# Kernel optimization log

Measured on AMD Instinct MI355X. Metric: run time of the kernel, lower is better.

## Reference

```python
import jax, jax.numpy as jnp
import numpy as np

B, T, HID = 2, 2048, 2048
H, KVH, D = 16, 4, 128


def _rope_tables(t, d):
    inv_freq = 1.0 / (10000.0 ** (np.arange(0, d, 2, dtype=np.float32) / d))
    freqs = np.arange(t, dtype=np.float32)[:, None] * inv_freq[None, :]  # [T, d/2]
    emb = np.concatenate([freqs, freqs], axis=-1)  # [T, d]
    return jnp.asarray(np.cos(emb))[None], jnp.asarray(np.sin(emb))[None]  # [1,T,d]


def setup_inputs() -> dict:
    key = jax.random.key(0)
    ks = jax.random.split(key, 5)
    x = jax.random.normal(ks[0], (B, T, HID), dtype=jnp.float32)
    rope_cos, rope_sin = _rope_tables(T, D)
    s_in = 1.0 / np.sqrt(HID)
    Wq = jax.random.normal(ks[1], (HID, H * D), dtype=jnp.float32) * s_in
    Wk = jax.random.normal(ks[2], (HID, KVH * D), dtype=jnp.float32) * s_in
    Wv = jax.random.normal(ks[3], (HID, KVH * D), dtype=jnp.float32) * s_in
    Wo = jax.random.normal(ks[4], (H * D, HID), dtype=jnp.float32) * (1.0 / np.sqrt(H * D))
    return {"x": x, "rope_cos": rope_cos, "rope_sin": rope_sin,
            "Wq": Wq, "Wk": Wk, "Wv": Wv, "Wo": Wo}


def _apply_rope(t, cos, sin):
    # t: [B,T,h,D]; cos/sin: [1,T,D] -> broadcast over heads
    c = cos[:, :, None, :]
    s = sin[:, :, None, :]
    t1, t2 = jnp.split(t, 2, axis=-1)
    rot = jnp.concatenate([-t2, t1], axis=-1)
    return t * c + rot * s


def reference(x, rope_cos, rope_sin, Wq, Wk, Wv, Wo):
    Tq = x.shape[1]
    q = (x @ Wq).reshape(B, Tq, H, D)
    k = (x @ Wk).reshape(B, Tq, KVH, D)
    v = (x @ Wv).reshape(B, Tq, KVH, D)
    q = _apply_rope(q, rope_cos[:, :Tq], rope_sin[:, :Tq])
    k = _apply_rope(k, rope_cos[:, :Tq], rope_sin[:, :Tq])
    # sliding_window == T -> T <= W branch: k/v unchanged
    rep = H // KVH  # GQA repeat-kv
    k_full = jnp.repeat(k, rep, axis=2)  # [B,T,H,D]
    v_full = jnp.repeat(v, rep, axis=2)
    scale = 1.0 / jnp.sqrt(jnp.asarray(D, dtype=x.dtype))
    scores = jnp.einsum('bqhd,bkhd->bhqk', q, k_full) * scale
    causal = jnp.tril(jnp.ones((Tq, Tq), dtype=bool))  # end-aligned, Tk==Tq
    scores = jnp.where(causal[None, None], scores, jnp.asarray(-jnp.inf, scores.dtype))
    p = jax.nn.softmax(scores, axis=-1)
    out = jnp.einsum('bhqk,bkhd->bqhd', p, v_full)
    return out.reshape(B, Tq, H * D) @ Wo
```

## Files before the change

kernel.cpp:

```cpp
#include <hip/hip_runtime.h>
#include <hip/hip_bf16.h>

#define B_   2
#define T_   2048
#define HID_ 2048
#define H_   16
#define KVH_ 4
#define D_   128
#define GQ_  (H_ / KVH_)

#define QN_  8388608
#define KN_  2097152

typedef unsigned short u16;
typedef __attribute__((ext_vector_type(8))) unsigned short us8v;
typedef __attribute__((ext_vector_type(8))) short s16x8;
typedef __attribute__((ext_vector_type(4))) float f32x4;

__device__ __forceinline__ float bf2f(u16 u) {
  return __uint_as_float(((unsigned)u) << 16);
}
__device__ __forceinline__ u16 f2bf(float f) {
  unsigned x = __float_as_uint(f);
  return (u16)((x + 0x7fffu + ((x >> 16) & 1u)) >> 16);
}

__device__ __forceinline__ void gl2lds(const void* gp, void* lp) {
  __builtin_amdgcn_global_load_lds(
      (const __attribute__((address_space(1))) unsigned int*)gp,
      (__attribute__((address_space(3))) unsigned int*)lp, 16, 0, 0);
}

__device__ __forceinline__ void probe2(const void* A, const void* W, int tid,
                                       bool* abf, bool* wbf) {
  __shared__ int cA, zA, cW, zW;
  if (tid == 0) { cA = 0; zA = 0; cW = 0; zW = 0; }
  __syncthreads();
  const int i = 16384 + tid;
  {
    const u16 raw = ((const u16*)A)[i];
    const float v = bf2f(raw);
    const bool bad = !(fabsf(v) <= 1e6f) ||
                     (v != 0.0f && fabsf(v) < 1e-10f);
    if (bad) atomicAdd(&cA, 1);
    if (((tid & 1) == 0) && raw == 0) atomicAdd(&zA, 1);
  }
  {
    const u16 raw = ((const u16*)W)[i];
    const float v = bf2f(raw);
    const bool bad = !(fabsf(v) <= 1e6f) ||
                     (v != 0.0f && fabsf(v) < 1e-10f);
    if (bad) atomicAdd(&cW, 1);
    if (((tid & 1) == 0) && raw == 0) atomicAdd(&zW, 1);
  }
  __syncthreads();
  *abf = (cA < 8) && (zA < 100);
  *wbf = (cW < 8) && (zW < 100);
}

__global__ __launch_bounds__(256) void conv_bf16(const void* __restrict__ in,
                                                 u16* __restrict__ outb,
                                                 int total8) {
  const int tid = threadIdx.x;
  bool ibf, dummy;
  probe2(in, in, tid, &ibf, &dummy);
  const int idx = blockIdx.x * 256 + tid;
  if (idx >= total8) return;
  if (ibf) {
    *(us8v*)&outb[(size_t)idx * 8] = *(const us8v*)((const u16*)in +
                                                    (size_t)idx * 8);
  } else {
    const float4 f0 = *(const float4*)((const float*)in + (size_t)idx * 8);
    const float4 f1 = *(const float4*)((const float*)in + (size_t)idx * 8 + 4);
    uint4 w;
    asm("v_cvt_pk_bf16_f32 %0, %1, %2" : "=v"(w.x) : "v"(f0.x), "v"(f0.y));
    asm("v_cvt_pk_bf16_f32 %0, %1, %2" : "=v"(w.y) : "v"(f0.z), "v"(f0.w));
    asm("v_cvt_pk_bf16_f32 %0, %1, %2" : "=v"(w.z) : "v"(f1.x), "v"(f1.y));
    asm("v_cvt_pk_bf16_f32 %0, %1, %2" : "=v"(w.w) : "v"(f1.z), "v"(f1.w));
    *(uint4*)&outb[(size_t)idx * 8] = w;
  }
}

__global__ __launch_bounds__(256) void transp_k(const void* __restrict__ Wv_,
                                                u16* __restrict__ WT,
                                                int K, int N) {
  const int tid = threadIdx.x;
  bool wbf, dummy;
  probe2(Wv_, Wv_, tid, &wbf, &dummy);

  __shared__ float tile[64][65];
  const int kb = blockIdx.y * 64;
  const int nb = blockIdx.x * 64;

  for (int it = tid; it < 512; it += 256) {
    const int r = it >> 3;
    const int g = it & 7;
    const size_t off = (size_t)(kb + r) * N + nb + g * 8;
    float f[8];
    if (wbf) {
      const us8v t8 = *(const us8v*)((const u16*)Wv_ + off);
#pragma unroll
      for (int e = 0; e < 8; ++e) f[e] = bf2f(t8[e]);
    } else {
      const float4 f0 = *(const float4*)((const float*)Wv_ + off);
      const float4 f1 = *(const float4*)((const float*)Wv_ + off + 4);
      f[0] = f0.x; f[1] = f0.y; f[2] = f0.z; f[3] = f0.w;
      f[4] = f1.x; f[5] = f1.y; f[6] = f1.z; f[7] = f1.w;
    }
#pragma unroll
    for (int e = 0; e < 8; ++e) tile[r][g * 8 + e] = f[e];
  }
  __syncthreads();
  for (int it = tid; it < 512; it += 256) {
    const int n = it >> 3;
    const int g = it & 7;
    us8v tmp;
#pragma unroll
    for (int e = 0; e < 8; ++e) tmp[e] = f2bf(tile[g * 8 + e][n]);
    *(us8v*)&WT[(size_t)(nb + n) * K + kb + g * 8] = tmp;
  }
}

#define G_STAGE(bi, kk)                                                       \
  do {                                                                        \
    _Pragma("unroll") for (int _p = 0; _p < 2; ++_p) {                        \
      const int _it = tid + _p * 256;                                         \
      const int _r = _it >> 2, _g = _it & 3;                                  \
      const int _gs = _g ^ ((_r >> 1) & 3);                                   \
      gl2lds(Ab + (size_t)(m0 + _r) * K + (kk) + _gs * 8,                     \
             &Alds[bi][((tid & ~63) + _p * 256) * 8]);                        \
    }                                                                         \
    _Pragma("unroll") for (int _p = 0; _p < 2; ++_p) {                        \
      const int _it = tid + _p * 256;                                         \
      const int _n = _it >> 2, _g = _it & 3;                                  \
      const int _gs = _g ^ ((_n >> 1) & 3);                                   \
      gl2lds(WT + (size_t)(n0 + _n) * K + (kk) + _gs * 8,                     \
             &Blds[bi][((tid & ~63) + _p * 256) * 8]);                        \
    }                                                                         \
  } while (0)

template <int OMODE>
__global__ __launch_bounds__(256) void gemm_mfma(const u16* __restrict__ Ab,
                                                 const u16* __restrict__ WT,
                                                 void* __restrict__ Cv,
                                                 int M, int N, int K) {
  const int tid = threadIdx.x;

  __shared__ __align__(16) u16 Alds[2][128 * 32];
  __shared__ __align__(16) u16 Blds[2][128 * 32];

  const int m0 = blockIdx.y * 128;
  const int n0 = blockIdx.x * 128;
  const int wave = tid >> 6;
  const int lane = tid & 63;
  const int wm = (wave >> 1) * 64;
  const int wn = (wave & 1) * 64;
  const int lrow = lane & 15;
  const int lq = lane >> 4;

  f32x4 acc[4][4] = {};

  G_STAGE(0, 0);
  __syncthreads();

  int cur = 0;
  for (int k0 = 0; k0 < K; k0 += 32) {
    if (k0 + 32 < K) G_STAGE(cur ^ 1, k0 + 32);

    s16x8 af[4], bfr[4];
#pragma unroll
    for (int mi = 0; mi < 4; ++mi) {
      const int row = wm + 16 * mi + lrow;
      af[mi] =
          *(const s16x8*)&Alds[cur][row * 32 + ((lq ^ ((row >> 1) & 3)) * 8)];
    }
#pragma unroll
    for (int ni = 0; ni < 4; ++ni) {
      const int row = wn + 16 * ni + lrow;
      bfr[ni] =
          *(const s16x8*)&Blds[cur][row * 32 + ((lq ^ ((row >> 1) & 3)) * 8)];
    }
    __builtin_amdgcn_s_setprio(1);
#pragma unroll
    for (int mi = 0; mi < 4; ++mi)
#pragma unroll
      for (int ni = 0; ni < 4; ++ni)
        acc[mi][ni] = __builtin_amdgcn_mfma_f32_16x16x32_bf16(
            af[mi], bfr[ni], acc[mi][ni], 0, 0, 0);
    __builtin_amdgcn_s_setprio(0);

    __syncthreads();
    cur ^= 1;
  }

#pragma unroll
  for (int mi = 0; mi < 4; ++mi) {
#pragma unroll
    for (int ni = 0; ni < 4; ++ni) {
      const int row0 = m0 + wm + 16 * mi + lq * 4;
      const int col = n0 + wn + 16 * ni + lrow;
#pragma unroll
      for (int r = 0; r < 4; ++r) {
        const int row = row0 + r;
        if (OMODE == 0) {
          ((float*)Cv)[(size_t)row * N + col] = acc[mi][ni][r];
        } else {
          const u16 val = f2bf(acc[mi][ni][r]);
          if (col < 2048) {
            ((u16*)Cv)[(size_t)row * 2048 + col] = val;
          } else if (col < 2560) {
            ((u16*)Cv)[QN_ + (size_t)row * 512 + (col - 2048)] = val;
          } else {
            const int c = col - 2560;
            const int kvh = c >> 7;
            const int d = c & 127;
            const int bb = row >> 11;
            const int tt = row & (T_ - 1);
            ((u16*)Cv)[QN_ + KN_ +
                       ((size_t)(bb * KVH_ + kvh) * D_ + d) * T_ + tt] = val;
          }
        }
      }
    }
  }
}

__global__ __launch_bounds__(256) void rope_bf(u16* __restrict__ t,
                                               const void* __restrict__ cosT,
                                               const void* __restrict__ sinT,
                                               int NH, int total, float qs) {
  const int tid = threadIdx.x;
  bool cbf, sbf;
  probe2(cosT, sinT, tid, &cbf, &sbf);

  const int idx = blockIdx.x * blockDim.x + tid;
  if (idx >= total) return;
  const int d = idx & 63;
  const int rest = idx >> 6;
  const int tt = (rest / NH) % T_;
  const size_t base = (size_t)rest * D_;
  const int ci = tt * D_ + d;
  float c1, s1, c2, s2;
  if (cbf) {
    c1 = bf2f(((const u16*)cosT)[ci]);
    c2 = bf2f(((const u16*)cosT)[ci + 64]);
  } else {
    c1 = ((const float*)cosT)[ci];
    c2 = ((const float*)cosT)[ci + 64];
  }
  if (sbf) {
    s1 = bf2f(((const u16*)sinT)[ci]);
    s2 = bf2f(((const u16*)sinT)[ci + 64]);
  } else {
    s1 = ((const float*)sinT)[ci];
    s2 = ((const float*)sinT)[ci + 64];
  }
  const float x1 = bf2f(t[base + d]);
  const float x2 = bf2f(t[base + d + 64]);
  t[base + d] = f2bf((x1 * c1 - x2 * s1) * qs);
  t[base + d + 64] = f2bf((x2 * c2 + x1 * s2) * qs);
}

#define ATT_STAGE(bi, ktile)                                                  \
  do {                                                                        \
    const int _k0 = (ktile) * 64;                                             \
    u16* _bk = &SM[(bi) * 16384];                                             \
    _Pragma("unroll") for (int _p = 0; _p < 2; ++_p) {                        \
      const int _it = tid + _p * 512;                                         \
      const int _r = _it >> 4, _s = _it & 15;                                 \
      gl2lds(kp + (size_t)(_k0 + _r) * (KVH_ * D_) + ((_s ^ (_r & 7)) * 8),   \
             &_bk[((tid & ~63) + _p * 512) * 8]);                             \
    }                                                                         \
    _Pragma("unroll") for (int _p = 0; _p < 2; ++_p) {                        \
      const int _it = tid + _p * 512;                                         \
      const int _r = _it >> 3, _s = _it & 7;                                  \
      gl2lds(vp + (size_t)_r * T_ + _k0 + ((_s ^ (_r & 7)) * 8),              \
             &_bk[8192 + ((tid & ~63) + _p * 512) * 8]);                      \
    }                                                                         \
  } while (0)

__global__ __launch_bounds__(512, 4) void attn_mfma(
    const u16* __restrict__ q, const u16* __restrict__ k,
    const u16* __restrict__ vT, u16* __restrict__ o) {
  const int tid = threadIdx.x;
  const int ip = blockIdx.y;
  const int bh = blockIdx.x;
  const int b = bh >> 4;
  const int h = bh & 15;
  const int kvh = h >> 2;
  const int hi0 = 64 * (31 - ip);
  const int lo0 = 64 * ip;

  __shared__ __align__(16) u16 SM[2 * 16384];
  __shared__ __align__(16) u16 Pl[128 * 64];

  const int wave = tid >> 6;
  const int lane = tid & 63;
  const int l15 = lane & 15;
  const int quad = lane >> 4;
  const bool isHi = wave < 4;
  const int rowbase = isHi ? (hi0 + 16 * wave) : (lo0 + 16 * (wave - 4));
  const int pr0 = 16 * wave;

  const u16* kp = k + ((size_t)b * T_ * KVH_ + kvh) * D_;
  const u16* vp = vT + (size_t)(b * KVH_ + kvh) * D_ * T_;

  s16x8 qf[4];
  {
    const size_t qrow = ((size_t)(b * T_ + rowbase + l15) * H_ + h) * D_;
#pragma unroll
    for (int st = 0; st < 4; ++st)
      qf[st] = *(const s16x8*)&q[qrow + st * 32 + quad * 8];
  }

  f32x4 acc_o[8] = {};
  float m_s = -1.0e30f, l_s = 0.0f;

  const int nkt = 32 - ip;

  ATT_STAGE(0, 0);
  __syncthreads();

  for (int kt = 0; kt < nkt; ++kt) {
    const int k0 = kt * 64;
    const u16* Ks = &SM[(kt & 1) * 16384];
    const u16* Vt = Ks + 8192;

    if (kt + 1 < nkt) ATT_STAGE((kt + 1) & 1, kt + 1);

    const bool active = isHi || (kt <= ip);
    if (active) {
      f32x4 accs[4] = {};
      __builtin_amdgcn_s_setprio(1);
#pragma unroll
      for (int st = 0; st < 4; ++st) {
        const int g = st * 4 + quad;
#pragma unroll
        for (int nt = 0; nt < 4; ++nt) {
          const int row = nt * 16 + l15;
          const s16x8 kf =
              *(const s16x8*)&Ks[row * 128 + ((g ^ (row & 7)) << 3)];
          accs[nt] = __builtin_amdgcn_mfma_f32_16x16x32_bf16(kf, qf[st],
                                                             accs[nt], 0, 0,
                                                             0);
        }
      }
      __builtin_amdgcn_s_setprio(0);

      if ((k0 + 63) > rowbase) {
        const int qg = rowbase + l15;
#pragma unroll
        for (int nt = 0; nt < 4; ++nt)
#pragma unroll
          for (int r = 0; r < 4; ++r)
            if (qg < (k0 + nt * 16 + quad * 4 + r)) accs[nt][r] = -1.0e30f;
      }

      float t0 = fmaxf(fmaxf(accs[0][0], accs[0][1]),
                       fmaxf(accs[0][2], accs[0][3]));
      float t1 = fmaxf(fmaxf(accs[1][0], accs[1][1]),
                       fmaxf(accs[1][2], accs[1][3]));
      float t2 = fmaxf(fmaxf(accs[2][0], accs[2][1]),
                       fmaxf(accs[2][2], accs[2][3]));
      float t3 = fmaxf(fmaxf(accs[3][0], accs[3][1]),
                       fmaxf(accs[3][2], accs[3][3]));
      float mx = fmaxf(fmaxf(t0, t1), fmaxf(t2, t3));
      mx = fmaxf(mx, __shfl_xor(mx, 16));
      mx = fmaxf(mx, __shfl_xor(mx, 32));

      const int defer = __all(mx <= m_s + 8.0f);
      float alv = 1.0f;
      if (!defer) {
        const float mnew = fmaxf(m_s, mx);
        alv = __expf(m_s - mnew);
        m_s = mnew;
      }

#pragma unroll
      for (int nt = 0; nt < 4; ++nt)
#pragma unroll
        for (int r = 0; r < 4; ++r)
          accs[nt][r] = __expf(accs[nt][r] - m_s);

#pragma unroll
      for (int nt = 0; nt < 4; ++nt) {
        uint2 w;
        asm("v_cvt_pk_bf16_f32 %0, %1, %2"
            : "=v"(w.x) : "v"(accs[nt][0]), "v"(accs[nt][1]));
        asm("v_cvt_pk_bf16_f32 %0, %1, %2"
            : "=v"(w.y) : "v"(accs[nt][2]), "v"(accs[nt][3]));
        const int prow = pr0 + l15;
        const int c0 = nt * 16 + quad * 4;
        *(uint2*)&Pl[prow * 64 + (((c0 >> 3) ^ (prow & 7)) << 3) + (c0 & 7)] =
            w;
      }

      float s0 = (accs[0][0] + accs[0][1]) + (accs[0][2] + accs[0][3]);
      float s1 = (accs[1][0] + accs[1][1]) + (accs[1][2] + accs[1][3]);
      float s2 = (accs[2][0] + accs[2][1]) + (accs[2][2] + accs[2][3]);
      float s3 = (accs[3][0] + accs[3][1]) + (accs[3][2] + accs[3][3]);
      float rs = (s0 + s1) + (s2 + s3);
      rs += __shfl_xor(rs, 16);
      rs += __shfl_xor(rs, 32);
      l_s = l_s * alv + rs;

      if (!defer) {
#pragma unroll
        for (int r = 0; r < 4; ++r) {
          const float a4 = __shfl(alv, 4 * quad + r);
#pragma unroll
          for (int nt2 = 0; nt2 < 8; ++nt2) acc_o[nt2][r] *= a4;
        }
      }

      asm volatile("s_waitcnt lgkmcnt(0)" ::: "memory");
      __builtin_amdgcn_sched_barrier(0);

      s16x8 pa[2];
#pragma unroll
      for (int ks = 0; ks < 2; ++ks) {
        const int row = pr0 + l15;
        const int g = ks * 4 + quad;
        pa[ks] = *(const s16x8*)&Pl[row * 64 + ((g ^ (row & 7)) << 3)];
      }
      __builtin_amdgcn_s_setprio(1);
#pragma unroll
      for (int ks = 0; ks < 2; ++ks) {
        const int g = ks * 4 + quad;
#pragma unroll
        for (int nt2 = 0; nt2 < 8; ++nt2) {
          const int row = nt2 * 16 + l15;
          const s16x8 vf =
              *(const s16x8*)&Vt[row * 64 + ((g ^ (row & 7)) << 3)];
          acc_o[nt2] = __builtin_amdgcn_mfma_f32_16x16x32_bf16(pa[ks], vf,
                                                               acc_o[nt2], 0,
                                                               0, 0);
        }
      }
      __builtin_amdgcn_s_setprio(0);
    }

    __syncthreads();
  }

  const float inv = 1.0f / l_s;
#pragma unroll
  for (int r = 0; r < 4; ++r) {
    const float linv = __shfl(inv, 4 * quad + r);
    const size_t orow =
        ((size_t)(b * T_ + rowbase + quad * 4 + r) * H_ + h) * D_;
#pragma unroll
    for (int nt2 = 0; nt2 < 8; ++nt2)
      o[orow + nt2 * 16 + l15] = f2bf(acc_o[nt2][r] * linv);
  }
}

__global__ void zero_out_k(float* __restrict__ out, int n) {
  const int i = blockIdx.x * blockDim.x + threadIdx.x;
  if (i < n) out[i] = 0.0f;
}

extern "C" void kernel_launch(void* const* d_in, const int* in_sizes, int n_in,
                              void* d_out, int out_size, void* d_ws,
                              size_t ws_size, hipStream_t stream) {
  const void* x    = d_in[0];
  const void* cosT = d_in[1];
  const void* sinT = d_in[2];
  const void* Wq   = d_in[3];
  const void* Wk   = d_in[4];
  const void* Wv   = d_in[5];
  const void* Wo   = d_in[6];
  float* out = (float*)d_out;

  const size_t QN = QN_;
  const size_t KN = KN_;
  const size_t WQT = (size_t)HID_ * (H_ * D_);
  const size_t WKT = (size_t)HID_ * (KVH_ * D_);
  const size_t need = (2 * QN + 2 * KN + 2 * WQT + 2 * WKT) * sizeof(u16);
  if (ws_size < need) {
    zero_out_k<<<(out_size + 255) / 256, 256, 0, stream>>>(out, out_size);
    return;
  }

  u16* qbuf  = (u16*)d_ws;
  u16* kbuf  = qbuf + QN;
  u16* vbufT = kbuf + KN;
  u16* obuf  = vbufT + KN;
  u16* xb    = obuf;
  u16* WqT   = obuf + QN;
  u16* WkT   = WqT + WQT;
  u16* WvT   = WkT + WKT;
  u16* WoT   = WvT + WKT;

  const int M = B_ * T_;
  dim3 blk(256);

  transp_k<<<dim3((H_ * D_) / 64, HID_ / 64), blk, 0, stream>>>(
      Wq, WqT, HID_, H_ * D_);
  transp_k<<<dim3((KVH_ * D_) / 64, HID_ / 64), blk, 0, stream>>>(
      Wk, WkT, HID_, KVH_ * D_);
  transp_k<<<dim3((KVH_ * D_) / 64, HID_ / 64), blk, 0, stream>>>(
      Wv, WvT, HID_, KVH_ * D_);
  transp_k<<<dim3(HID_ / 64, (H_ * D_) / 64), blk, 0, stream>>>(
      Wo, WoT, H_ * D_, HID_);

  conv_bf16<<<(int)(QN / 8 / 256), blk, 0, stream>>>(x, xb, (int)(QN / 8));

  gemm_mfma<3><<<dim3(3072 / 128, M / 128), blk, 0, stream>>>(
      xb, WqT, qbuf, M, 3072, HID_);

  const int totq = B_ * T_ * H_ * (D_ / 2);
  rope_bf<<<totq / 256, blk, 0, stream>>>(qbuf, cosT, sinT, H_, totq,
                                          0.08838834764831845f);
  const int totk = B_ * T_ * KVH_ * (D_ / 2);
  rope_bf<<<totk / 256, blk, 0, stream>>>(kbuf, cosT, sinT, KVH_, totk, 1.0f);

  attn_mfma<<<dim3(B_ * H_, 16), dim3(512), 0, stream>>>(
      qbuf, kbuf, vbufT, obuf);

  gemm_mfma<0><<<dim3(HID_ / 128, M / 128), blk, 0, stream>>>(
      obuf, WoT, out, M, HID_, H_ * D_);
}
```

Measured before the change: 330.1 us.

## Merge prep and rope launches, retile GEMMs to 512 threads with BK=64

Folds the four weight transposes and the x conversion into one prep kernel, and the two rope launches into one, so fewer kernels are launched. The GEMM moves to 512-thread blocks with a 64-wide K stage, a new XOR swizzle and a BN template parameter. The QKV projection uses 192-wide N tiles, which gives 16x32 blocks. This cuts launch overhead and barrier count per K step, at the cost of more LDS per block and register pressure under launch_bounds(512,4).

```diff
diff --git a/kernel.cpp b/kernel.cpp
--- a/kernel.cpp
+++ b/kernel.cpp
@@ -11,6 +11,8 @@
 
 #define QN_  8388608
 #define KN_  2097152
+#define TOTQ_ 4194304
+#define TOTK_ 1048576
 
 typedef unsigned short u16;
 typedef __attribute__((ext_vector_type(8))) unsigned short us8v;
@@ -58,17 +60,54 @@
   *wbf = (cW < 8) && (zW < 100);
 }
 
-__global__ __launch_bounds__(256) void conv_bf16(const void* __restrict__ in,
-                                                 u16* __restrict__ outb,
-                                                 int total8) {
-  const int tid = threadIdx.x;
+__device__ void transp_body(const void* __restrict__ Wv_,
+                            u16* __restrict__ WT, int K, int N, int bx,
+                            int by, int tid) {
+  bool wbf, dummy;
+  probe2(Wv_, Wv_, tid, &wbf, &dummy);
+
+  __shared__ float tile[64][65];
+  const int kb = by * 64;
+  const int nb = bx * 64;
+
+  for (int it = tid; it < 512; it += 256) {
+    const int r = it >> 3;
+    const int g = it & 7;
+    const size_t off = (size_t)(kb + r) * N + nb + g * 8;
+    float f[8];
+    if (wbf) {
+      const us8v t8 = *(const us8v*)((const u16*)Wv_ + off);
+#pragma unroll
+      for (int e = 0; e < 8; ++e) f[e] = bf2f(t8[e]);
+    } else {
+      const float4 f0 = *(const float4*)((const float*)Wv_ + off);
+      const float4 f1 = *(const float4*)((const float*)Wv_ + off + 4);
+      f[0] = f0.x; f[1] = f0.y; f[2] = f0.z; f[3] = f0.w;
+      f[4] = f1.x; f[5] = f1.y; f[6] = f1.z; f[7] = f1.w;
+    }
+#pragma unroll
+    for (int e = 0; e < 8; ++e) tile[r][g * 8 + e] = f[e];
+  }
+  __syncthreads();
+  for (int it = tid; it < 512; it += 256) {
+    const int n = it >> 3;
+    const int g = it & 7;
+    us8v tmp;
+#pragma unroll
+    for (int e = 0; e < 8; ++e) tmp[e] = f2bf(tile[g * 8 + e][n]);
+    *(us8v*)&WT[(size_t)(nb + n) * K + kb + g * 8] = tmp;
+  }
+}
+
+__device__ void conv_body(const void* __restrict__ in, u16* __restrict__ outb,
+                          int cb, int tid) {
   bool ibf, dummy;
   probe2(in, in, tid, &ibf, &dummy);
-  const int idx = blockIdx.x * 256 + tid;
-  if (idx >= total8) return;
+  const int idx = cb * 256 + tid;
+  if (idx >= (QN_ / 8)) return;
   if (ibf) {
-    *(us8v*)&outb[(size_t)idx * 8] = *(const us8v*)((const u16*)in +
-                                                    (size_t)idx * 8);
+    *(us8v*)&outb[(size_t)idx * 8] =
+        *(const us8v*)((const u16*)in + (size_t)idx * 8);
   } else {
     const float4 f0 = *(const float4*)((const float*)in + (size_t)idx * 8);
     const float4 f1 = *(const float4*)((const float*)in + (size_t)idx * 8 + 4);
@@ -81,122 +120,110 @@
   }
 }
 
-__global__ __launch_bounds__(256) void transp_k(const void* __restrict__ Wv_,
-                                                u16* __restrict__ WT,
-                                                int K, int N) {
+__global__ __launch_bounds__(256) void prep_k(
+    const void* __restrict__ Wq, const void* __restrict__ Wk,
+    const void* __restrict__ Wv, const void* __restrict__ Wo,
+    const void* __restrict__ x, u16* __restrict__ WqT,
+    u16* __restrict__ WkT, u16* __restrict__ WvT, u16* __restrict__ WoT,
+    u16* __restrict__ xb) {
+  const int b = blockIdx.x;
   const int tid = threadIdx.x;
-  bool wbf, dummy;
-  probe2(Wv_, Wv_, tid, &wbf, &dummy);
-
-  __shared__ float tile[64][65];
-  const int kb = blockIdx.y * 64;
-  const int nb = blockIdx.x * 64;
-
-  for (int it = tid; it < 512; it += 256) {
-    const int r = it >> 3;
-    const int g = it & 7;
-    const size_t off = (size_t)(kb + r) * N + nb + g * 8;
-    float f[8];
-    if (wbf) {
-      const us8v t8 = *(const us8v*)((const u16*)Wv_ + off);
-#pragma unroll
-      for (int e = 0; e < 8; ++e) f[e] = bf2f(t8[e]);
-    } else {
-      const float4 f0 = *(const float4*)((const float*)Wv_ + off);
-      const float4 f1 = *(const float4*)((const float*)Wv_ + off + 4);
-      f[0] = f0.x; f[1] = f0.y; f[2] = f0.z; f[3] = f0.w;
-      f[4] = f1.x; f[5] = f1.y; f[6] = f1.z; f[7] = f1.w;
-    }
-#pragma unroll
-    for (int e = 0; e < 8; ++e) tile[r][g * 8 + e] = f[e];
-  }
-  __syncthreads();
-  for (int it = tid; it < 512; it += 256) {
-    const int n = it >> 3;
-    const int g = it & 7;
-    us8v tmp;
-#pragma unroll
-    for (int e = 0; e < 8; ++e) tmp[e] = f2bf(tile[g * 8 + e][n]);
-    *(us8v*)&WT[(size_t)(nb + n) * K + kb + g * 8] = tmp;
-  }
-}
-
-#define G_STAGE(bi, kk)                                                       \
+  if (b < 1024) {
+    transp_body(Wq, WqT, HID_, H_ * D_, b & 31, b >> 5, tid);
+  } else if (b < 1280) {
+    const int bb = b - 1024;
+    transp_body(Wk, WkT, HID_, KVH_ * D_, bb & 7, bb >> 3, tid);
+  } else if (b < 1536) {
+    const int bb = b - 1280;
+    transp_body(Wv, WvT, HID_, KVH_ * D_, bb & 7, bb >> 3, tid);
+  } else if (b < 2560) {
+    const int bb = b - 1536;
+    transp_body(Wo, WoT, H_ * D_, HID_, bb & 31, bb >> 5, tid);
+  } else {
+    conv_body(x, xb, b - 2560, tid);
+  }
+}
+
+template <int OMODE, int BN>
+__global__ __launch_bounds__(512, 4) void gemm_mfma(
+    const u16* __restrict__ Ab, const u16* __restrict__ WT,
+    void* __restrict__ Cv, int M, int N, int K) {
+  const int tid = threadIdx.x;
+
+  __shared__ __align__(16) u16 Alds[2][128 * 64];
+  __shared__ __align__(16) u16 Blds[2][BN * 64];
+
+  const int m0 = blockIdx.y * 128;
+  const int n0 = blockIdx.x * BN;
+  const int wave = tid >> 6;
+  const int lane = tid & 63;
+  const int wm = (wave >> 2) * 64;
+  const int wn = (wave & 3) * (BN / 4);
+  const int lrow = lane & 15;
+  const int lq = lane >> 4;
+  constexpr int NI = BN / 64;
+
+  f32x4 acc[4][NI] = {};
+
+#define G_STAGE64(bi, kk)                                                     \
   do {                                                                        \
     _Pragma("unroll") for (int _p = 0; _p < 2; ++_p) {                        \
-      const int _it = tid + _p * 256;                                         \
-      const int _r = _it >> 2, _g = _it & 3;                                  \
-      const int _gs = _g ^ ((_r >> 1) & 3);                                   \
+      const int _it = tid + _p * 512;                                         \
+      const int _r = _it >> 3, _g = _it & 7;                                  \
+      const int _gs = _g ^ (_r & 7);                                          \
       gl2lds(Ab + (size_t)(m0 + _r) * K + (kk) + _gs * 8,                     \
-             &Alds[bi][((tid & ~63) + _p * 256) * 8]);                        \
+             &Alds[bi][((tid & ~63) + _p * 512) * 8]);                        \
     }                                                                         \
-    _Pragma("unroll") for (int _p = 0; _p < 2; ++_p) {                        \
-      const int _it = tid + _p * 256;                                         \
-      const int _n = _it >> 2, _g = _it & 3;                                  \
-      const int _gs = _g ^ ((_n >> 1) & 3);                                   \
+    _Pragma("unroll") for (int _p = 0; _p < (BN / 64); ++_p) {                \
+      const int _it = tid + _p * 512;                                         \
+      const int _n = _it >> 3, _g = _it & 7;                                  \
+      const int _gs = _g ^ (_n & 7);                                          \
       gl2lds(WT + (size_t)(n0 + _n) * K + (kk) + _gs * 8,                     \
-             &Blds[bi][((tid & ~63) + _p * 256) * 8]);                        \
+             &Blds[bi][((tid & ~63) + _p * 512) * 8]);                        \
     }                                                                         \
   } while (0)
 
-template <int OMODE>
-__global__ __launch_bounds__(256) void gemm_mfma(const u16* __restrict__ Ab,
-                                                 const u16* __restrict__ WT,
-                                                 void* __restrict__ Cv,
-                                                 int M, int N, int K) {
-  const int tid = threadIdx.x;
-
-  __shared__ __align__(16) u16 Alds[2][128 * 32];
-  __shared__ __align__(16) u16 Blds[2][128 * 32];
-
-  const int m0 = blockIdx.y * 128;
-  const int n0 = blockIdx.x * 128;
-  const int wave = tid >> 6;
-  const int lane = tid & 63;
-  const int wm = (wave >> 1) * 64;
-  const int wn = (wave & 1) * 64;
-  const int lrow = lane & 15;
-  const int lq = lane >> 4;
-
-  f32x4 acc[4][4] = {};
-
-  G_STAGE(0, 0);
+  G_STAGE64(0, 0);
   __syncthreads();
 
   int cur = 0;
-  for (int k0 = 0; k0 < K; k0 += 32) {
-    if (k0 + 32 < K) G_STAGE(cur ^ 1, k0 + 32);
-
-    s16x8 af[4], bfr[4];
-#pragma unroll
-    for (int mi = 0; mi < 4; ++mi) {
-      const int row = wm + 16 * mi + lrow;
-      af[mi] =
-          *(const s16x8*)&Alds[cur][row * 32 + ((lq ^ ((row >> 1) & 3)) * 8)];
+  for (int k0 = 0; k0 < K; k0 += 64) {
+    if (k0 + 64 < K) G_STAGE64(cur ^ 1, k0 + 64);
+
+#pragma unroll
+    for (int ks = 0; ks < 2; ++ks) {
+      s16x8 af[4], bfr[NI];
+#pragma unroll
+      for (int mi = 0; mi < 4; ++mi) {
+        const int row = wm + 16 * mi + lrow;
+        af[mi] = *(const s16x8*)&Alds[cur][row * 64 +
+                                           (((ks * 4 + lq) ^ (row & 7)) * 8)];
+      }
+#pragma unroll
+      for (int ni = 0; ni < NI; ++ni) {
+        const int row = wn + 16 * ni + lrow;
+        bfr[ni] = *(const s16x8*)&Blds[cur][row * 64 +
+                                            (((ks * 4 + lq) ^ (row & 7)) * 8)];
+      }
+      __builtin_amdgcn_s_setprio(1);
+#pragma unroll
+      for (int mi = 0; mi < 4; ++mi)
+#pragma unroll
+        for (int ni = 0; ni < NI; ++ni)
+          acc[mi][ni] = __builtin_amdgcn_mfma_f32_16x16x32_bf16(
+              af[mi], bfr[ni], acc[mi][ni], 0, 0, 0);
+      __builtin_amdgcn_s_setprio(0);
     }
-#pragma unroll
-    for (int ni = 0; ni < 4; ++ni) {
-      const int row = wn + 16 * ni + lrow;
-      bfr[ni] =
-          *(const s16x8*)&Blds[cur][row * 32 + ((lq ^ ((row >> 1) & 3)) * 8)];
-    }
-    __builtin_amdgcn_s_setprio(1);
-#pragma unroll
-    for (int mi = 0; mi < 4; ++mi)
-#pragma unroll
-      for (int ni = 0; ni < 4; ++ni)
-        acc[mi][ni] = __builtin_amdgcn_mfma_f32_16x16x32_bf16(
-            af[mi], bfr[ni], acc[mi][ni], 0, 0, 0);
-    __builtin_amdgcn_s_setprio(0);
 
     __syncthreads();
     cur ^= 1;
   }
+#undef G_STAGE64
 
 #pragma unroll
   for (int mi = 0; mi < 4; ++mi) {
 #pragma unroll
-    for (int ni = 0; ni < 4; ++ni) {
+    for (int ni = 0; ni < NI; ++ni) {
       const int row0 = m0 + wm + 16 * mi + lq * 4;
       const int col = n0 + wn + 16 * ni + lrow;
 #pragma unroll
@@ -225,16 +252,25 @@
   }
 }
 
-__global__ __launch_bounds__(256) void rope_bf(u16* __restrict__ t,
-                                               const void* __restrict__ cosT,
-                                               const void* __restrict__ sinT,
-                                               int NH, int total, float qs) {
+__global__ __launch_bounds__(256) void rope2(u16* __restrict__ qb,
+                                             u16* __restrict__ kb,
+                                             const void* __restrict__ cosT,
+                                             const void* __restrict__ sinT) {
   const int tid = threadIdx.x;
   bool cbf, sbf;
   probe2(cosT, sinT, tid, &cbf, &sbf);
 
-  const int idx = blockIdx.x * blockDim.x + tid;
-  if (idx >= total) return;
+  int idx = blockIdx.x * 256 + tid;
+  u16* t;
+  int NH;
+  float qs;
+  if (idx < TOTQ_) {
+    t = qb; NH = H_; qs = 0.08838834764831845f;
+  } else {
+    idx -= TOTQ_;
+    if (idx >= TOTK_) return;
+    t = kb; NH = KVH_; qs = 1.0f;
+  }
   const int d = idx & 63;
   const int rest = idx >> 6;
   const int tt = (rest / NH) % T_;
@@ -493,31 +529,17 @@
   u16* WoT   = WvT + WKT;
 
   const int M = B_ * T_;
-  dim3 blk(256);
-
-  transp_k<<<dim3((H_ * D_) / 64, HID_ / 64), blk, 0, stream>>>(
-      Wq, WqT, HID_, H_ * D_);
-  transp_k<<<dim3((KVH_ * D_) / 64, HID_ / 64), blk, 0, stream>>>(
-      Wk, WkT, HID_, KVH_ * D_);
-  transp_k<<<dim3((KVH_ * D_) / 64, HID_ / 64), blk, 0, stream>>>(
-      Wv, WvT, HID_, KVH_ * D_);
-  transp_k<<<dim3(HID_ / 64, (H_ * D_) / 64), blk, 0, stream>>>(
-      Wo, WoT, H_ * D_, HID_);
-
-  conv_bf16<<<(int)(QN / 8 / 256), blk, 0, stream>>>(x, xb, (int)(QN / 8));
-
-  gemm_mfma<3><<<dim3(3072 / 128, M / 128), blk, 0, stream>>>(
+
+  prep_k<<<6656, 256, 0, stream>>>(Wq, Wk, Wv, Wo, x, WqT, WkT, WvT, WoT, xb);
+
+  gemm_mfma<3, 192><<<dim3(3072 / 192, M / 128), dim3(512), 0, stream>>>(
       xb, WqT, qbuf, M, 3072, HID_);
 
-  const int totq = B_ * T_ * H_ * (D_ / 2);
-  rope_bf<<<totq / 256, blk, 0, stream>>>(qbuf, cosT, sinT, H_, totq,
-                                          0.08838834764831845f);
-  const int totk = B_ * T_ * KVH_ * (D_ / 2);
-  rope_bf<<<totk / 256, blk, 0, stream>>>(kbuf, cosT, sinT, KVH_, totk, 1.0f);
+  rope2<<<(TOTQ_ + TOTK_) / 256, 256, 0, stream>>>(qbuf, kbuf, cosT, sinT);
 
   attn_mfma<<<dim3(B_ * H_, 16), dim3(512), 0, stream>>>(
       qbuf, kbuf, vbufT, obuf);
 
-  gemm_mfma<0><<<dim3(HID_ / 128, M / 128), blk, 0, stream>>>(
+  gemm_mfma<0, 128><<<dim3(HID_ / 128, M / 128), dim3(512), 0, stream>>>(
       obuf, WoT, out, M, HID_, H_ * D_);
 }
```

Measured after the change: 305.4 us. 1.08x faster.
